# Kernel optimization log

Hardware: AMD Instinct MI355X
Metric: run time of the kernel (lower is better)

## Reference

```python
import jax, jax.numpy as jnp
import numpy as np

B, L, D, H, HD = 4, 1024, 768, 12, 64

def setup_inputs() -> dict:
    key = jax.random.key(0)
    ks = jax.random.split(key, 8)
    s = 0.02
    return {
        "x": jax.random.normal(ks[0], (B, L, D), dtype=jnp.float32),
        "Wq": jax.random.normal(ks[1], (D, H * HD), dtype=jnp.float32) * s,
        "Wk": jax.random.normal(ks[2], (D, H * HD), dtype=jnp.float32) * s,
        "Wv": jax.random.normal(ks[3], (D, H * HD), dtype=jnp.float32) * s,
        "pre_attn": jax.random.normal(ks[4], (H, H), dtype=jnp.float32),
        "post_attn": jax.random.normal(ks[5], (H, H), dtype=jnp.float32),
        "Wo": jax.random.normal(ks[6], (H * HD, D), dtype=jnp.float32) * s,
        "bo": jnp.zeros((D,), dtype=jnp.float32),
    }

def reference(x, Wq, Wk, Wv, pre_attn, post_attn, Wo, bo):
    b, l, _ = x.shape
    # projections (no bias)
    q = x @ Wq  # [B, L, H*HD]
    k = x @ Wk
    v = x @ Wv
    # split heads: b l (h d) -> b h l d
    split = lambda t: t.reshape(b, l, H, HD).transpose(0, 2, 1, 3)
    qh, kh, vh = split(q), split(k), split(v)
    scale = 1.0 / jnp.sqrt(jnp.float32(HD))
    a = jnp.einsum('bhid,bhjd->bhij', qh, kh) * scale  # [B,H,L,L]
    # talking-heads: pre-softmax mix, softmax, post-softmax mix
    a = jnp.einsum('bhij,hg->bgij', a, pre_attn)
    a = jax.nn.softmax(a, axis=-1)
    a = jnp.einsum('bhij,hg->bgij', a, post_attn)
    av = jnp.einsum('bhij,bhjd->bhid', a, vh)  # [B,H,L,HD]
    # faithful to original: raw reshape of [(b h), l, d] -> [b, l, h*d]
    # (row-major, mixes h and l axes exactly like torch .reshape)
    av = av.reshape(b, l, H * HD)
    return av @ Wo + bo
```

## Files before the change

kernel.cpp:

```cpp
#include <hip/hip_runtime.h>

#define D_MODEL 768
#define NHEAD   12
#define HDIM    64
#define SEQ     1024
#define BATCH   4
#define QBLK    16
#define KVBLK   64
#define NT      (SEQ / KVBLK)

typedef __attribute__((ext_vector_type(8))) short short8v;
typedef __attribute__((ext_vector_type(4))) float f32x4;

__device__ __forceinline__ ushort f2bf(float f) {
    union { float f; unsigned u; } c; c.f = f;
    unsigned r = c.u + 0x7fffu + ((c.u >> 16) & 1u);
    return (ushort)(r >> 16);
}

__global__ void cast_bf16_kernel(const float* __restrict__ src,
                                 ushort* __restrict__ dst, int n4)
{
    int idx = blockIdx.x * blockDim.x + threadIdx.x;
    if (idx >= n4) return;
    float4 v = ((const float4*)src)[idx];
    ushort4 o;
    o.x = f2bf(v.x); o.y = f2bf(v.y); o.z = f2bf(v.z); o.w = f2bf(v.w);
    ((ushort4*)dst)[idx] = o;
}

__global__ __launch_bounds__(256) void castT4_kernel(
    const float* __restrict__ W0, const float* __restrict__ W1,
    const float* __restrict__ W2, const float* __restrict__ W3,
    ushort* __restrict__ D0, ushort* __restrict__ D1,
    ushort* __restrict__ D2, ushort* __restrict__ D3)
{
    __shared__ float tile[32][33];
    const int z = blockIdx.z;
    const float* W = (z == 0) ? W0 : (z == 1) ? W1 : (z == 2) ? W2 : W3;
    ushort*     D = (z == 0) ? D0 : (z == 1) ? D1 : (z == 2) ? D2 : D3;

    const int kb  = blockIdx.x * 32;
    const int nb  = blockIdx.y * 32;
    const int tid = threadIdx.x;
    const int r   = tid >> 3;
    const int c4  = (tid & 7) * 4;

    float4 v = *(const float4*)(W + (size_t)(kb + r) * 768 + nb + c4);
    tile[r][c4 + 0] = v.x; tile[r][c4 + 1] = v.y;
    tile[r][c4 + 2] = v.z; tile[r][c4 + 3] = v.w;
    __syncthreads();

    ushort4 o;
    o.x = f2bf(tile[c4 + 0][r]);
    o.y = f2bf(tile[c4 + 1][r]);
    o.z = f2bf(tile[c4 + 2][r]);
    o.w = f2bf(tile[c4 + 3][r]);
    *(ushort4*)(D + (size_t)(nb + r) * 768 + kb + c4) = o;
}

template<int BF16OUT>
__global__ __launch_bounds__(256) void gemm_bf16_kernel(
    const ushort* __restrict__ A, const ushort* __restrict__ BT,
    void* __restrict__ C0v, void* __restrict__ C1v, void* __restrict__ C2v,
    const float* __restrict__ bias, ushort* __restrict__ VT)
{
    __shared__ __align__(16) ushort As[128 * 32];
    __shared__ __align__(16) ushort Bs[128 * 32];

    const int bm  = blockIdx.x * 128;
    const int bnG = blockIdx.y * 128;
    const int sel = bnG / 768;
    void* Cv = (sel == 0) ? C0v : ((sel == 1) ? C1v : C2v);
    const int ncol0 = bnG - sel * 768;

    const int tid  = threadIdx.x;
    const int lane = tid & 63;
    const int wave = tid >> 6;
    const int wm = wave >> 1, wn = wave & 1;

    f32x4 acc[4][4];
    #pragma unroll
    for (int i = 0; i < 4; i++)
        #pragma unroll
        for (int j = 0; j < 4; j++)
            acc[i][j] = (f32x4){0.f, 0.f, 0.f, 0.f};

    const int sr = tid >> 2;
    const int sk = (tid & 3) * 8;
    const ushort* Ap = A  + (size_t)(bm  + sr) * 768 + sk;
    const ushort* Bp = BT + (size_t)(bnG + sr) * 768 + sk;
    char* AsDst = (char*)As + tid * 16;
    char* BsDst = (char*)Bs + tid * 16;

    for (int k0 = 0; k0 < 768; k0 += 32) {
        __syncthreads();
        __builtin_amdgcn_global_load_lds(
            (const __attribute__((address_space(1))) void*)(Ap + k0),
            (__attribute__((address_space(3))) void*)AsDst, 16, 0, 0);
        __builtin_amdgcn_global_load_lds(
            (const __attribute__((address_space(1))) void*)(Ap + (size_t)64 * 768 + k0),
            (__attribute__((address_space(3))) void*)(AsDst + 4096), 16, 0, 0);
        __builtin_amdgcn_global_load_lds(
            (const __attribute__((address_space(1))) void*)(Bp + k0),
            (__attribute__((address_space(3))) void*)BsDst, 16, 0, 0);
        __builtin_amdgcn_global_load_lds(
            (const __attribute__((address_space(1))) void*)(Bp + (size_t)64 * 768 + k0),
            (__attribute__((address_space(3))) void*)(BsDst + 4096), 16, 0, 0);
        __syncthreads();

        short8v a[4], b[4];
        #pragma unroll
        for (int i = 0; i < 4; i++)
            a[i] = *(const short8v*)((const char*)As +
                     (wm * 64 + i * 16 + (lane & 15)) * 64 + (lane >> 4) * 16);
        #pragma unroll
        for (int j = 0; j < 4; j++)
            b[j] = *(const short8v*)((const char*)Bs +
                     (wn * 64 + j * 16 + (lane & 15)) * 64 + (lane >> 4) * 16);
        #pragma unroll
        for (int i = 0; i < 4; i++)
            #pragma unroll
            for (int j = 0; j < 4; j++)
                acc[i][j] = __builtin_amdgcn_mfma_f32_16x16x32_bf16(a[i], b[j], acc[i][j], 0, 0, 0);
    }

    const int cc = lane & 15, cr = lane >> 4;
    if (BF16OUT && VT != nullptr && sel == 2) {
        #pragma unroll
        for (int j = 0; j < 4; j++) {
            const int hcol = ncol0 + wn * 64 + j * 16 + cc;
            const int h2 = hcol >> 6, dd = hcol & 63;
            #pragma unroll
            for (int i = 0; i < 4; i++) {
                const int row0 = bm + wm * 64 + i * 16 + cr * 4;
                const int bb = row0 >> 10, jj = row0 & 1023;
                ushort4 o;
                o.x = f2bf(acc[i][j][0]); o.y = f2bf(acc[i][j][1]);
                o.z = f2bf(acc[i][j][2]); o.w = f2bf(acc[i][j][3]);
                *(ushort4*)(VT + (((size_t)bb * NHEAD + h2) * HDIM + dd) * SEQ + jj) = o;
            }
        }
        return;
    }
    #pragma unroll
    for (int j = 0; j < 4; j++) {
        const int col = ncol0 + wn * 64 + j * 16 + cc;
        const float badd = bias ? bias[col] : 0.f;
        #pragma unroll
        for (int i = 0; i < 4; i++) {
            #pragma unroll
            for (int r = 0; r < 4; r++) {
                const int row = bm + wm * 64 + i * 16 + cr * 4 + r;
                if (BF16OUT)
                    ((ushort*)Cv)[(size_t)row * 768 + col] = f2bf(acc[i][j][r] + badd);
                else
                    ((float*)Cv)[(size_t)row * 768 + col] = acc[i][j][r] + badd;
            }
        }
    }
}

__global__ __launch_bounds__(768, 1) void attn_mfma_kernel(
    const ushort* __restrict__ qb, const ushort* __restrict__ kb,
    const ushort* __restrict__ vt, const float* __restrict__ pre_attn,
    const float* __restrict__ post_attn, ushort* __restrict__ avb)
{
    __shared__ __align__(16) float sA[NHEAD][QBLK][68];
    __shared__ __align__(16) float sE[NHEAD][QBLK][68];
    __shared__ float pre_l[NHEAD * NHEAD];
    __shared__ float post_l[NHEAD * NHEAD];
    __shared__ float l_lds[NHEAD][QBLK];

    const int i0  = blockIdx.x * QBLK;
    const int b   = blockIdx.y;
    const int tid = threadIdx.x;
    const int lane = tid & 63;
    const int h    = tid >> 6;

    if (tid < 144) pre_l[tid] = pre_attn[tid] * (0.125f * 1.44269504f);
    else if (tid < 288) post_l[tid - 144] = post_attn[tid - 144];

    const int lr = lane & 15;
    const int lc = lane >> 4;

    const ushort* qbase = qb + ((size_t)b * SEQ + i0 + lr) * D_MODEL + h * HDIM + lc * 8;
    const short8v a_q0 = *(const short8v*)(qbase);
    const short8v a_q1 = *(const short8v*)(qbase + 32);

    const ushort* kbase  = kb + ((size_t)b * SEQ + lr) * D_MODEL + h * HDIM + lc * 8;
    const ushort* vtbase = vt + (((size_t)b * NHEAD + h) * HDIM + lr) * SEQ + lc * 8;

    float lsum = 0.f;
    for (int t = 0; t < NT; t++) {
        const int j0 = t * KVBLK;
        float (*S)[QBLK][68] = (t & 1) ? sE : sA;

        f32x4 sf[4];
        #pragma unroll
        for (int cf = 0; cf < 4; cf++) {
            const ushort* kp = kbase + (size_t)(j0 + cf * 16) * D_MODEL;
            short8v bk0 = *(const short8v*)(kp);
            short8v bk1 = *(const short8v*)(kp + 32);
            f32x4 a = (f32x4){0.f, 0.f, 0.f, 0.f};
            a = __builtin_amdgcn_mfma_f32_16x16x32_bf16(a_q0, bk0, a, 0, 0, 0);
            a = __builtin_amdgcn_mfma_f32_16x16x32_bf16(a_q1, bk1, a, 0, 0, 0);
            sf[cf] = a;
        }
        #pragma unroll
        for (int cf = 0; cf < 4; cf++)
            #pragma unroll
            for (int rr = 0; rr < 4; rr++)
                S[h][lc * 4 + rr][cf * 16 + lr] = sf[cf][rr];
        __syncthreads();

        float mix[16];
        #pragma unroll
        for (int c = 0; c < 16; c++) mix[c] = 0.f;
        #pragma unroll
        for (int hh = 0; hh < NHEAD; hh++) {
            const float w = pre_l[hh * NHEAD + h];
            const float* row = &S[hh][lr][0];
            const float4 a0 = *(const float4*)(row + lc * 8);
            const float4 a1 = *(const float4*)(row + lc * 8 + 4);
            const float4 a2 = *(const float4*)(row + 32 + lc * 8);
            const float4 a3 = *(const float4*)(row + 36 + lc * 8);
            mix[0]  = fmaf(a0.x, w, mix[0]);  mix[1]  = fmaf(a0.y, w, mix[1]);
            mix[2]  = fmaf(a0.z, w, mix[2]);  mix[3]  = fmaf(a0.w, w, mix[3]);
            mix[4]  = fmaf(a1.x, w, mix[4]);  mix[5]  = fmaf(a1.y, w, mix[5]);
            mix[6]  = fmaf(a1.z, w, mix[6]);  mix[7]  = fmaf(a1.w, w, mix[7]);
            mix[8]  = fmaf(a2.x, w, mix[8]);  mix[9]  = fmaf(a2.y, w, mix[9]);
            mix[10] = fmaf(a2.z, w, mix[10]); mix[11] = fmaf(a2.w, w, mix[11]);
            mix[12] = fmaf(a3.x, w, mix[12]); mix[13] = fmaf(a3.y, w, mix[13]);
            mix[14] = fmaf(a3.z, w, mix[14]); mix[15] = fmaf(a3.w, w, mix[15]);
        }
        #pragma unroll
        for (int c = 0; c < 16; c++) lsum += exp2f(mix[c]);
    }
    float lrow = lsum;
    lrow += __shfl_xor(lrow, 16);
    lrow += __shfl_xor(lrow, 32);
    if (lc == 0) l_lds[h][lr] = lrow;
    __syncthreads();

    float il[NHEAD];
    #pragma unroll
    for (int hh = 0; hh < NHEAD; hh++) il[hh] = 1.f / l_lds[hh][lr];

    f32x4 o_acc[4];
    #pragma unroll
    for (int d = 0; d < 4; d++) o_acc[d] = (f32x4){0.f, 0.f, 0.f, 0.f};

    for (int t = 0; t < NT; t++) {
        const int j0 = t * KVBLK;

        f32x4 sf[4];
        #pragma unroll
        for (int cf = 0; cf < 4; cf++) {
            const ushort* kp = kbase + (size_t)(j0 + cf * 16) * D_MODEL;
            short8v bk0 = *(const short8v*)(kp);
            short8v bk1 = *(const short8v*)(kp + 32);
            f32x4 a = (f32x4){0.f, 0.f, 0.f, 0.f};
            a = __builtin_amdgcn_mfma_f32_16x16x32_bf16(a_q0, bk0, a, 0, 0, 0);
            a = __builtin_amdgcn_mfma_f32_16x16x32_bf16(a_q1, bk1, a, 0, 0, 0);
            sf[cf] = a;
        }
        #pragma unroll
        for (int cf = 0; cf < 4; cf++)
            #pragma unroll
            for (int rr = 0; rr < 4; rr++)
                sA[h][lc * 4 + rr][cf * 16 + lr] = sf[cf][rr];
        __syncthreads();

        float mix[16];
        #pragma unroll
        for (int c = 0; c < 16; c++) mix[c] = 0.f;
        #pragma unroll
        for (int hh = 0; hh < NHEAD; hh++) {
            const float w = pre_l[hh * NHEAD + h];
            const float* row = &sA[hh][lr][0];
            const float4 a0 = *(const float4*)(row + lc * 8);
            const float4 a1 = *(const float4*)(row + lc * 8 + 4);
            const float4 a2 = *(const float4*)(row + 32 + lc * 8);
            const float4 a3 = *(const float4*)(row + 36 + lc * 8);
            mix[0]  = fmaf(a0.x, w, mix[0]);  mix[1]  = fmaf(a0.y, w, mix[1]);
            mix[2]  = fmaf(a0.z, w, mix[2]);  mix[3]  = fmaf(a0.w, w, mix[3]);
            mix[4]  = fmaf(a1.x, w, mix[4]);  mix[5]  = fmaf(a1.y, w, mix[5]);
            mix[6]  = fmaf(a1.z, w, mix[6]);  mix[7]  = fmaf(a1.w, w, mix[7]);
            mix[8]  = fmaf(a2.x, w, mix[8]);  mix[9]  = fmaf(a2.y, w, mix[9]);
            mix[10] = fmaf(a2.z, w, mix[10]); mix[11] = fmaf(a2.w, w, mix[11]);
            mix[12] = fmaf(a3.x, w, mix[12]); mix[13] = fmaf(a3.y, w, mix[13]);
            mix[14] = fmaf(a3.z, w, mix[14]); mix[15] = fmaf(a3.w, w, mix[15]);
        }
        float e[16];
        #pragma unroll
        for (int c = 0; c < 16; c++) e[c] = exp2f(mix[c]);

        {
            float* row = &sE[h][lr][0];
            *(float4*)(row + lc * 8)      = *(float4*)(&e[0]);
            *(float4*)(row + lc * 8 + 4)  = *(float4*)(&e[4]);
            *(float4*)(row + 32 + lc * 8) = *(float4*)(&e[8]);
            *(float4*)(row + 36 + lc * 8) = *(float4*)(&e[12]);
        }
        __syncthreads();

        float pm[16];
        #pragma unroll
        for (int c = 0; c < 16; c++) pm[c] = 0.f;
        #pragma unroll
        for (int hh = 0; hh < NHEAD; hh++) {
            const float w = post_l[hh * NHEAD + h] * il[hh];
            const float* row = &sE[hh][lr][0];
            const float4 a0 = *(const float4*)(row + lc * 8);
            const float4 a1 = *(const float4*)(row + lc * 8 + 4);
            const float4 a2 = *(const float4*)(row + 32 + lc * 8);
            const float4 a3 = *(const float4*)(row + 36 + lc * 8);
            pm[0]  = fmaf(a0.x, w, pm[0]);  pm[1]  = fmaf(a0.y, w, pm[1]);
            pm[2]  = fmaf(a0.z, w, pm[2]);  pm[3]  = fmaf(a0.w, w, pm[3]);
            pm[4]  = fmaf(a1.x, w, pm[4]);  pm[5]  = fmaf(a1.y, w, pm[5]);
            pm[6]  = fmaf(a1.z, w, pm[6]);  pm[7]  = fmaf(a1.w, w, pm[7]);
            pm[8]  = fmaf(a2.x, w, pm[8]);  pm[9]  = fmaf(a2.y, w, pm[9]);
            pm[10] = fmaf(a2.z, w, pm[10]); pm[11] = fmaf(a2.w, w, pm[11]);
            pm[12] = fmaf(a3.x, w, pm[12]); pm[13] = fmaf(a3.y, w, pm[13]);
            pm[14] = fmaf(a3.z, w, pm[14]); pm[15] = fmaf(a3.w, w, pm[15]);
        }
        short8v pa0, pa1;
        #pragma unroll
        for (int c = 0; c < 8; c++) {
            ((ushort*)&pa0)[c] = f2bf(pm[c]);
            ((ushort*)&pa1)[c] = f2bf(pm[8 + c]);
        }

        #pragma unroll
        for (int d = 0; d < 4; d++) {
            short8v bv0 = *(const short8v*)(vtbase + (size_t)(d * 16) * SEQ + j0);
            short8v bv1 = *(const short8v*)(vtbase + (size_t)(d * 16) * SEQ + j0 + 32);
            o_acc[d] = __builtin_amdgcn_mfma_f32_16x16x32_bf16(pa0, bv0, o_acc[d], 0, 0, 0);
            o_acc[d] = __builtin_amdgcn_mfma_f32_16x16x32_bf16(pa1, bv1, o_acc[d], 0, 0, 0);
        }
    }

    #pragma unroll
    for (int d = 0; d < 4; d++)
        #pragma unroll
        for (int rr = 0; rr < 4; rr++)
            avb[(((size_t)b * NHEAD + h) * SEQ + i0 + lc * 4 + rr) * HDIM + d * 16 + lr]
                = f2bf(o_acc[d][rr]);
}

extern "C" void kernel_launch(void* const* d_in, const int* in_sizes, int n_in,
                              void* d_out, int out_size, void* d_ws, size_t ws_size,
                              hipStream_t stream)
{
    const float* x    = (const float*)d_in[0];
    const float* Wq   = (const float*)d_in[1];
    const float* Wk   = (const float*)d_in[2];
    const float* Wv   = (const float*)d_in[3];
    const float* pre  = (const float*)d_in[4];
    const float* post = (const float*)d_in[5];
    const float* Wo   = (const float*)d_in[6];
    const float* bo   = (const float*)d_in[7];
    float* out = (float*)d_out;

    const size_t SZ = (size_t)BATCH * SEQ * D_MODEL;
    ushort* qbf    = (ushort*)d_ws;
    ushort* kbf    = qbf + SZ;
    ushort* vt     = kbf + SZ;
    ushort* xb_avb = vt  + SZ;
    ushort* qkvT   = xb_avb + SZ;
    ushort* WoT    = qkvT + (size_t)2304 * 768;

    cast_bf16_kernel<<<(int)(SZ / 4 + 255) / 256, 256, 0, stream>>>(x, xb_avb, (int)(SZ / 4));
    castT4_kernel<<<dim3(24, 24, 4), 256, 0, stream>>>(
        Wq, Wk, Wv, Wo,
        qkvT, qkvT + (size_t)768 * 768, qkvT + (size_t)2 * 768 * 768, WoT);

    gemm_bf16_kernel<1><<<dim3(32, 18), 256, 0, stream>>>(
        xb_avb, qkvT, qbf, kbf, nullptr, nullptr, vt);

    attn_mfma_kernel<<<dim3(SEQ / QBLK, BATCH), 768, 0, stream>>>(
        qbf, kbf, vt, pre, post, xb_avb);

    gemm_bf16_kernel<0><<<dim3(32, 6), 256, 0, stream>>>(
        xb_avb, WoT, out, out, out, bo, nullptr);
}
```

Before: 377.1 us.

## Restructure talking-heads mixing so each thread mixes all heads for one score

Scores are now stored in LDS head-interleaved (13-float stride per position), so each thread reads all 12 head values for one (row, key) pair and does the pre-mix, exp and post-mix entirely in registers. This removes the second LDS round trip for the exp values and one barrier per tile. The probabilities are then written to a bf16 LDS tile for the PV MFMA. The block grows to 16 waves so that all 16 query rows get a wave, but only 12 waves issue MFMAs, and the per-head row sums now need a full-wave shuffle reduction.

Result: faster. 343.0 us (-9.0%).

```diff
diff --git a/kernel.cpp b/kernel.cpp
--- a/kernel.cpp
+++ b/kernel.cpp
@@ -8,6 +8,7 @@
 #define QBLK    16
 #define KVBLK   64
 #define NT      (SEQ / KVBLK)
+#define SPITCH  834
 
 typedef __attribute__((ext_vector_type(8))) short short8v;
 typedef __attribute__((ext_vector_type(4))) float f32x4;
@@ -161,192 +162,182 @@
     }
 }
 
-__global__ __launch_bounds__(768, 1) void attn_mfma_kernel(
+__global__ __launch_bounds__(1024, 1) void attn_mfma_kernel(
     const ushort* __restrict__ qb, const ushort* __restrict__ kb,
     const ushort* __restrict__ vt, const float* __restrict__ pre_attn,
     const float* __restrict__ post_attn, ushort* __restrict__ avb)
 {
-    __shared__ __align__(16) float sA[NHEAD][QBLK][68];
-    __shared__ __align__(16) float sE[NHEAD][QBLK][68];
-    __shared__ float pre_l[NHEAD * NHEAD];
-    __shared__ float post_l[NHEAD * NHEAD];
+    __shared__ __align__(16) float S0[QBLK * SPITCH];
+    __shared__ __align__(16) float S1[QBLK * SPITCH];
+    __shared__ __align__(16) ushort P[NHEAD][QBLK][72];
+    __shared__ __align__(16) float prew[NHEAD][16];
+    __shared__ __align__(16) float postw[NHEAD][16];
     __shared__ float l_lds[NHEAD][QBLK];
 
     const int i0  = blockIdx.x * QBLK;
     const int b   = blockIdx.y;
     const int tid = threadIdx.x;
     const int lane = tid & 63;
-    const int h    = tid >> 6;
-
-    if (tid < 144) pre_l[tid] = pre_attn[tid] * (0.125f * 1.44269504f);
-    else if (tid < 288) post_l[tid - 144] = post_attn[tid - 144];
-
-    const int lr = lane & 15;
-    const int lc = lane >> 4;
-
-    const ushort* qbase = qb + ((size_t)b * SEQ + i0 + lr) * D_MODEL + h * HDIM + lc * 8;
-    const short8v a_q0 = *(const short8v*)(qbase);
-    const short8v a_q1 = *(const short8v*)(qbase + 32);
-
-    const ushort* kbase  = kb + ((size_t)b * SEQ + lr) * D_MODEL + h * HDIM + lc * 8;
-    const ushort* vtbase = vt + (((size_t)b * NHEAD + h) * HDIM + lr) * SEQ + lc * 8;
-
-    float lsum = 0.f;
+    const int w    = tid >> 6;
+
+    if (tid < 144) prew[tid / 12][tid % 12] = pre_attn[tid] * (0.125f * 1.44269504f);
+    else if (tid < 288) { int t2 = tid - 144; postw[t2 / 12][t2 % 12] = post_attn[t2]; }
+
+    const int lr = lane & 15, lc = lane >> 4;
+
+    short8v a_q0 = {0,0,0,0,0,0,0,0}, a_q1 = {0,0,0,0,0,0,0,0};
+    const ushort* kbase  = kb;
+    const ushort* vtbase = vt;
+    if (w < NHEAD) {
+        const ushort* qbase = qb + ((size_t)b * SEQ + i0 + lr) * D_MODEL + w * HDIM + lc * 8;
+        a_q0 = *(const short8v*)(qbase);
+        a_q1 = *(const short8v*)(qbase + 32);
+        kbase  = kb + ((size_t)b * SEQ + lr) * D_MODEL + w * HDIM + lc * 8;
+        vtbase = vt + (((size_t)b * NHEAD + w) * HDIM + lr) * SEQ + lc * 8;
+    }
+    __syncthreads();
+
+    float el[NHEAD];
+    #pragma unroll
+    for (int g = 0; g < NHEAD; g++) el[g] = 0.f;
+
+    for (int t = 0; t < NT; t++) {
+        float* S = (t & 1) ? S1 : S0;
+        if (w < NHEAD) {
+            const int j0 = t * KVBLK;
+            #pragma unroll
+            for (int cf = 0; cf < 4; cf++) {
+                const ushort* kp = kbase + (size_t)(j0 + cf * 16) * D_MODEL;
+                short8v bk0 = *(const short8v*)(kp);
+                short8v bk1 = *(const short8v*)(kp + 32);
+                f32x4 a = (f32x4){0.f, 0.f, 0.f, 0.f};
+                a = __builtin_amdgcn_mfma_f32_16x16x32_bf16(a_q0, bk0, a, 0, 0, 0);
+                a = __builtin_amdgcn_mfma_f32_16x16x32_bf16(a_q1, bk1, a, 0, 0, 0);
+                #pragma unroll
+                for (int rr = 0; rr < 4; rr++)
+                    S[(lc * 4 + rr) * SPITCH + (cf * 16 + lr) * 13 + w] = a[rr];
+            }
+        }
+        __syncthreads();
+
+        const float* sp = S + w * SPITCH + lane * 13;
+        float mv[NHEAD];
+        #pragma unroll
+        for (int g = 0; g < NHEAD; g++) mv[g] = 0.f;
+        #pragma unroll
+        for (int hh = 0; hh < NHEAD; hh++) {
+            const float s = sp[hh];
+            const float4 w0 = *(const float4*)&prew[hh][0];
+            const float4 w1 = *(const float4*)&prew[hh][4];
+            const float4 w2 = *(const float4*)&prew[hh][8];
+            mv[0] = fmaf(s, w0.x, mv[0]); mv[1]  = fmaf(s, w0.y, mv[1]);
+            mv[2] = fmaf(s, w0.z, mv[2]); mv[3]  = fmaf(s, w0.w, mv[3]);
+            mv[4] = fmaf(s, w1.x, mv[4]); mv[5]  = fmaf(s, w1.y, mv[5]);
+            mv[6] = fmaf(s, w1.z, mv[6]); mv[7]  = fmaf(s, w1.w, mv[7]);
+            mv[8] = fmaf(s, w2.x, mv[8]); mv[9]  = fmaf(s, w2.y, mv[9]);
+            mv[10] = fmaf(s, w2.z, mv[10]); mv[11] = fmaf(s, w2.w, mv[11]);
+        }
+        #pragma unroll
+        for (int g = 0; g < NHEAD; g++) el[g] += exp2f(mv[g]);
+    }
+
+    #pragma unroll
+    for (int g = 0; g < NHEAD; g++) {
+        float v = el[g];
+        v += __shfl_xor(v, 1);  v += __shfl_xor(v, 2);  v += __shfl_xor(v, 4);
+        v += __shfl_xor(v, 8);  v += __shfl_xor(v, 16); v += __shfl_xor(v, 32);
+        if (lane == 0) l_lds[g][w] = v;
+    }
+    __syncthreads();
+
+    float il[NHEAD];
+    #pragma unroll
+    for (int g = 0; g < NHEAD; g++) il[g] = 1.f / l_lds[g][w];
+
+    f32x4 o_acc[4];
+    #pragma unroll
+    for (int d = 0; d < 4; d++) o_acc[d] = (f32x4){0.f, 0.f, 0.f, 0.f};
+
     for (int t = 0; t < NT; t++) {
         const int j0 = t * KVBLK;
-        float (*S)[QBLK][68] = (t & 1) ? sE : sA;
-
-        f32x4 sf[4];
-        #pragma unroll
-        for (int cf = 0; cf < 4; cf++) {
-            const ushort* kp = kbase + (size_t)(j0 + cf * 16) * D_MODEL;
-            short8v bk0 = *(const short8v*)(kp);
-            short8v bk1 = *(const short8v*)(kp + 32);
-            f32x4 a = (f32x4){0.f, 0.f, 0.f, 0.f};
-            a = __builtin_amdgcn_mfma_f32_16x16x32_bf16(a_q0, bk0, a, 0, 0, 0);
-            a = __builtin_amdgcn_mfma_f32_16x16x32_bf16(a_q1, bk1, a, 0, 0, 0);
-            sf[cf] = a;
-        }
-        #pragma unroll
-        for (int cf = 0; cf < 4; cf++)
+        if (w < NHEAD) {
+            #pragma unroll
+            for (int cf = 0; cf < 4; cf++) {
+                const ushort* kp = kbase + (size_t)(j0 + cf * 16) * D_MODEL;
+                short8v bk0 = *(const short8v*)(kp);
+                short8v bk1 = *(const short8v*)(kp + 32);
+                f32x4 a = (f32x4){0.f, 0.f, 0.f, 0.f};
+                a = __builtin_amdgcn_mfma_f32_16x16x32_bf16(a_q0, bk0, a, 0, 0, 0);
+                a = __builtin_amdgcn_mfma_f32_16x16x32_bf16(a_q1, bk1, a, 0, 0, 0);
+                #pragma unroll
+                for (int rr = 0; rr < 4; rr++)
+                    S0[(lc * 4 + rr) * SPITCH + (cf * 16 + lr) * 13 + w] = a[rr];
+            }
+        }
+        __syncthreads();
+
+        const float* sp = S0 + w * SPITCH + lane * 13;
+        float mv[NHEAD];
+        #pragma unroll
+        for (int g = 0; g < NHEAD; g++) mv[g] = 0.f;
+        #pragma unroll
+        for (int hh = 0; hh < NHEAD; hh++) {
+            const float s = sp[hh];
+            const float4 w0 = *(const float4*)&prew[hh][0];
+            const float4 w1 = *(const float4*)&prew[hh][4];
+            const float4 w2 = *(const float4*)&prew[hh][8];
+            mv[0] = fmaf(s, w0.x, mv[0]); mv[1]  = fmaf(s, w0.y, mv[1]);
+            mv[2] = fmaf(s, w0.z, mv[2]); mv[3]  = fmaf(s, w0.w, mv[3]);
+            mv[4] = fmaf(s, w1.x, mv[4]); mv[5]  = fmaf(s, w1.y, mv[5]);
+            mv[6] = fmaf(s, w1.z, mv[6]); mv[7]  = fmaf(s, w1.w, mv[7]);
+            mv[8] = fmaf(s, w2.x, mv[8]); mv[9]  = fmaf(s, w2.y, mv[9]);
+            mv[10] = fmaf(s, w2.z, mv[10]); mv[11] = fmaf(s, w2.w, mv[11]);
+        }
+        #pragma unroll
+        for (int g = 0; g < NHEAD; g++) mv[g] = exp2f(mv[g]) * il[g];
+
+        float pm[NHEAD];
+        #pragma unroll
+        for (int g = 0; g < NHEAD; g++) pm[g] = 0.f;
+        #pragma unroll
+        for (int hh = 0; hh < NHEAD; hh++) {
+            const float s = mv[hh];
+            const float4 w0 = *(const float4*)&postw[hh][0];
+            const float4 w1 = *(const float4*)&postw[hh][4];
+            const float4 w2 = *(const float4*)&postw[hh][8];
+            pm[0] = fmaf(s, w0.x, pm[0]); pm[1]  = fmaf(s, w0.y, pm[1]);
+            pm[2] = fmaf(s, w0.z, pm[2]); pm[3]  = fmaf(s, w0.w, pm[3]);
+            pm[4] = fmaf(s, w1.x, pm[4]); pm[5]  = fmaf(s, w1.y, pm[5]);
+            pm[6] = fmaf(s, w1.z, pm[6]); pm[7]  = fmaf(s, w1.w, pm[7]);
+            pm[8] = fmaf(s, w2.x, pm[8]); pm[9]  = fmaf(s, w2.y, pm[9]);
+            pm[10] = fmaf(s, w2.z, pm[10]); pm[11] = fmaf(s, w2.w, pm[11]);
+        }
+        #pragma unroll
+        for (int g = 0; g < NHEAD; g++)
+            P[g][w][lane] = f2bf(pm[g]);
+        __syncthreads();
+
+        if (w < NHEAD) {
+            short8v pa0 = *(const short8v*)&P[w][lr][lc * 8];
+            short8v pa1 = *(const short8v*)&P[w][lr][lc * 8 + 32];
+            #pragma unroll
+            for (int d = 0; d < 4; d++) {
+                short8v bv0 = *(const short8v*)(vtbase + (size_t)(d * 16) * SEQ + j0);
+                short8v bv1 = *(const short8v*)(vtbase + (size_t)(d * 16) * SEQ + j0 + 32);
+                o_acc[d] = __builtin_amdgcn_mfma_f32_16x16x32_bf16(pa0, bv0, o_acc[d], 0, 0, 0);
+                o_acc[d] = __builtin_amdgcn_mfma_f32_16x16x32_bf16(pa1, bv1, o_acc[d], 0, 0, 0);
+            }
+        }
+    }
+
+    if (w < NHEAD) {
+        #pragma unroll
+        for (int d = 0; d < 4; d++)
             #pragma unroll
             for (int rr = 0; rr < 4; rr++)
-                S[h][lc * 4 + rr][cf * 16 + lr] = sf[cf][rr];
-        __syncthreads();
-
-        float mix[16];
-        #pragma unroll
-        for (int c = 0; c < 16; c++) mix[c] = 0.f;
-        #pragma unroll
-        for (int hh = 0; hh < NHEAD; hh++) {
-            const float w = pre_l[hh * NHEAD + h];
-            const float* row = &S[hh][lr][0];
-            const float4 a0 = *(const float4*)(row + lc * 8);
-            const float4 a1 = *(const float4*)(row + lc * 8 + 4);
-            const float4 a2 = *(const float4*)(row + 32 + lc * 8);
-            const float4 a3 = *(const float4*)(row + 36 + lc * 8);
-            mix[0]  = fmaf(a0.x, w, mix[0]);  mix[1]  = fmaf(a0.y, w, mix[1]);
-            mix[2]  = fmaf(a0.z, w, mix[2]);  mix[3]  = fmaf(a0.w, w, mix[3]);
-            mix[4]  = fmaf(a1.x, w, mix[4]);  mix[5]  = fmaf(a1.y, w, mix[5]);
-            mix[6]  = fmaf(a1.z, w, mix[6]);  mix[7]  = fmaf(a1.w, w, mix[7]);
-            mix[8]  = fmaf(a2.x, w, mix[8]);  mix[9]  = fmaf(a2.y, w, mix[9]);
-            mix[10] = fmaf(a2.z, w, mix[10]); mix[11] = fmaf(a2.w, w, mix[11]);
-            mix[12] = fmaf(a3.x, w, mix[12]); mix[13] = fmaf(a3.y, w, mix[13]);
-            mix[14] = fmaf(a3.z, w, mix[14]); mix[15] = fmaf(a3.w, w, mix[15]);
-        }
-        #pragma unroll
-        for (int c = 0; c < 16; c++) lsum += exp2f(mix[c]);
-    }
-    float lrow = lsum;
-    lrow += __shfl_xor(lrow, 16);
-    lrow += __shfl_xor(lrow, 32);
-    if (lc == 0) l_lds[h][lr] = lrow;
-    __syncthreads();
-
-    float il[NHEAD];
-    #pragma unroll
-    for (int hh = 0; hh < NHEAD; hh++) il[hh] = 1.f / l_lds[hh][lr];
-
-    f32x4 o_acc[4];
-    #pragma unroll
-    for (int d = 0; d < 4; d++) o_acc[d] = (f32x4){0.f, 0.f, 0.f, 0.f};
-
-    for (int t = 0; t < NT; t++) {
-        const int j0 = t * KVBLK;
-
-        f32x4 sf[4];
-        #pragma unroll
-        for (int cf = 0; cf < 4; cf++) {
-            const ushort* kp = kbase + (size_t)(j0 + cf * 16) * D_MODEL;
-            short8v bk0 = *(const short8v*)(kp);
-            short8v bk1 = *(const short8v*)(kp + 32);
-            f32x4 a = (f32x4){0.f, 0.f, 0.f, 0.f};
-            a = __builtin_amdgcn_mfma_f32_16x16x32_bf16(a_q0, bk0, a, 0, 0, 0);
-            a = __builtin_amdgcn_mfma_f32_16x16x32_bf16(a_q1, bk1, a, 0, 0, 0);
-            sf[cf] = a;
-        }
-        #pragma unroll
-        for (int cf = 0; cf < 4; cf++)
-            #pragma unroll
-            for (int rr = 0; rr < 4; rr++)
-                sA[h][lc * 4 + rr][cf * 16 + lr] = sf[cf][rr];
-        __syncthreads();
-
-        float mix[16];
-        #pragma unroll
-        for (int c = 0; c < 16; c++) mix[c] = 0.f;
-        #pragma unroll
-        for (int hh = 0; hh < NHEAD; hh++) {
-            const float w = pre_l[hh * NHEAD + h];
-            const float* row = &sA[hh][lr][0];
-            const float4 a0 = *(const float4*)(row + lc * 8);
-            const float4 a1 = *(const float4*)(row + lc * 8 + 4);
-            const float4 a2 = *(const float4*)(row + 32 + lc * 8);
-            const float4 a3 = *(const float4*)(row + 36 + lc * 8);
-            mix[0]  = fmaf(a0.x, w, mix[0]);  mix[1]  = fmaf(a0.y, w, mix[1]);
-            mix[2]  = fmaf(a0.z, w, mix[2]);  mix[3]  = fmaf(a0.w, w, mix[3]);
-            mix[4]  = fmaf(a1.x, w, mix[4]);  mix[5]  = fmaf(a1.y, w, mix[5]);
-            mix[6]  = fmaf(a1.z, w, mix[6]);  mix[7]  = fmaf(a1.w, w, mix[7]);
-            mix[8]  = fmaf(a2.x, w, mix[8]);  mix[9]  = fmaf(a2.y, w, mix[9]);
-            mix[10] = fmaf(a2.z, w, mix[10]); mix[11] = fmaf(a2.w, w, mix[11]);
-            mix[12] = fmaf(a3.x, w, mix[12]); mix[13] = fmaf(a3.y, w, mix[13]);
-            mix[14] = fmaf(a3.z, w, mix[14]); mix[15] = fmaf(a3.w, w, mix[15]);
-        }
-        float e[16];
-        #pragma unroll
-        for (int c = 0; c < 16; c++) e[c] = exp2f(mix[c]);
-
-        {
-            float* row = &sE[h][lr][0];
-            *(float4*)(row + lc * 8)      = *(float4*)(&e[0]);
-            *(float4*)(row + lc * 8 + 4)  = *(float4*)(&e[4]);
-            *(float4*)(row + 32 + lc * 8) = *(float4*)(&e[8]);
-            *(float4*)(row + 36 + lc * 8) = *(float4*)(&e[12]);
-        }
-        __syncthreads();
-
-        float pm[16];
-        #pragma unroll
-        for (int c = 0; c < 16; c++) pm[c] = 0.f;
-        #pragma unroll
-        for (int hh = 0; hh < NHEAD; hh++) {
-            const float w = post_l[hh * NHEAD + h] * il[hh];
-            const float* row = &sE[hh][lr][0];
-            const float4 a0 = *(const float4*)(row + lc * 8);
-            const float4 a1 = *(const float4*)(row + lc * 8 + 4);
-            const float4 a2 = *(const float4*)(row + 32 + lc * 8);
-            const float4 a3 = *(const float4*)(row + 36 + lc * 8);
-            pm[0]  = fmaf(a0.x, w, pm[0]);  pm[1]  = fmaf(a0.y, w, pm[1]);
-            pm[2]  = fmaf(a0.z, w, pm[2]);  pm[3]  = fmaf(a0.w, w, pm[3]);
-            pm[4]  = fmaf(a1.x, w, pm[4]);  pm[5]  = fmaf(a1.y, w, pm[5]);
-            pm[6]  = fmaf(a1.z, w, pm[6]);  pm[7]  = fmaf(a1.w, w, pm[7]);
-            pm[8]  = fmaf(a2.x, w, pm[8]);  pm[9]  = fmaf(a2.y, w, pm[9]);
-            pm[10] = fmaf(a2.z, w, pm[10]); pm[11] = fmaf(a2.w, w, pm[11]);
-            pm[12] = fmaf(a3.x, w, pm[12]); pm[13] = fmaf(a3.y, w, pm[13]);
-            pm[14] = fmaf(a3.z, w, pm[14]); pm[15] = fmaf(a3.w, w, pm[15]);
-        }
-        short8v pa0, pa1;
-        #pragma unroll
-        for (int c = 0; c < 8; c++) {
-            ((ushort*)&pa0)[c] = f2bf(pm[c]);
-            ((ushort*)&pa1)[c] = f2bf(pm[8 + c]);
-        }
-
-        #pragma unroll
-        for (int d = 0; d < 4; d++) {
-            short8v bv0 = *(const short8v*)(vtbase + (size_t)(d * 16) * SEQ + j0);
-            short8v bv1 = *(const short8v*)(vtbase + (size_t)(d * 16) * SEQ + j0 + 32);
-            o_acc[d] = __builtin_amdgcn_mfma_f32_16x16x32_bf16(pa0, bv0, o_acc[d], 0, 0, 0);
-            o_acc[d] = __builtin_amdgcn_mfma_f32_16x16x32_bf16(pa1, bv1, o_acc[d], 0, 0, 0);
-        }
-    }
-
-    #pragma unroll
-    for (int d = 0; d < 4; d++)
-        #pragma unroll
-        for (int rr = 0; rr < 4; rr++)
-            avb[(((size_t)b * NHEAD + h) * SEQ + i0 + lc * 4 + rr) * HDIM + d * 16 + lr]
-                = f2bf(o_acc[d][rr]);
+                avb[(((size_t)b * NHEAD + w) * SEQ + i0 + lc * 4 + rr) * HDIM + d * 16 + lr]
+                    = f2bf(o_acc[d][rr]);
+    }
 }
 
 extern "C" void kernel_launch(void* const* d_in, const int* in_sizes, int n_in,
@@ -379,7 +370,7 @@
     gemm_bf16_kernel<1><<<dim3(32, 18), 256, 0, stream>>>(
         xb_avb, qkvT, qbf, kbf, nullptr, nullptr, vt);
 
-    attn_mfma_kernel<<<dim3(SEQ / QBLK, BATCH), 768, 0, stream>>>(
+    attn_mfma_kernel<<<dim3(SEQ / QBLK, BATCH), 1024, 0, stream>>>(
         qbf, kbf, vt, pre, post, xb_avb);
 
     gemm_bf16_kernel<0><<<dim3(32, 6), 256, 0, stream>>>(
```
